# Performance work log

Measured on AMD Instinct MI355X. Metric: run time of the kernel, lower is better.

Reference implementation:

```python
import jax, jax.numpy as jnp
import numpy as np

H = 768   # hidden (cell) size
P = 256   # projection size
I = 80    # input feature dim
L = 3     # model_num_layers
B, T = 256, 400


def setup_inputs() -> dict:
    key = jax.random.key(0)
    ks = jax.random.split(key, 16)
    s = 0.05
    inp = {"x": jax.random.normal(ks[0], (B, T, I), dtype=jnp.float32)}
    in_dims = [I, P, P]
    for l in range(L):
        inp[f"Wx{l}"] = jax.random.normal(ks[1 + 4 * l], (in_dims[l], 4 * H), dtype=jnp.float32) * s
        inp[f"Wh{l}"] = jax.random.normal(ks[2 + 4 * l], (P, 4 * H), dtype=jnp.float32) * s
        inp[f"b{l}"] = jnp.zeros((4 * H,), dtype=jnp.float32)
        inp[f"Wp{l}"] = jax.random.normal(ks[3 + 4 * l], (H, P), dtype=jnp.float32) * s
    inp["W"] = jax.random.normal(ks[13], (P, P), dtype=jnp.float32) * s
    inp["lb"] = jnp.zeros((P,), dtype=jnp.float32)
    return inp


def _lstmp_layer(x, Wx, Wh, b, Wp, c0, h0):
    # Precompute input contribution to gates: [B, T, 4H]
    xg = jnp.einsum("bti,ig->btg", x, Wx) + b

    def step(carry, xg_t):
        c, h = carry
        gates = xg_t + h @ Wh              # [B, 4H]
        i, f, g, o = jnp.split(gates, 4, axis=-1)
        i = jax.nn.sigmoid(i)
        f = jax.nn.sigmoid(f)
        g = jnp.tanh(g)
        o = jax.nn.sigmoid(o)
        c = f * c + i * g                  # [B, H]
        h = (o * jnp.tanh(c)) @ Wp         # [B, P] projected hidden
        return (c, h), h

    (c, h), hs = jax.lax.scan(step, (c0, h0), jnp.swapaxes(xg, 0, 1))
    return jnp.swapaxes(hs, 0, 1), c, h   # seq_out [B,T,P], final c, h


def reference(x, Wx0, Wh0, b0, Wp0, Wx1, Wh1, b1, Wp1, Wx2, Wh2, b2, Wp2, W, lb):
    batch = x.shape[0]
    c = jnp.zeros((batch, H), dtype=x.dtype)
    h = jnp.zeros((batch, P), dtype=x.dtype)
    seq = x
    params = [(Wx0, Wh0, b0, Wp0), (Wx1, Wh1, b1, Wp1), (Wx2, Wh2, b2, Wp2)]
    for (Wx, Wh, b, Wp) in params:
        seq, c, h = _lstmp_layer(seq, Wx, Wh, b, Wp, c, h)
    embeds_raw = jax.nn.relu(seq.mean(axis=1) @ W.T + lb)   # [B, P]
    norm = jnp.linalg.norm(embeds_raw, axis=1, keepdims=True)
    return embeds_raw / norm
```

## Files before the change

### kernel.cpp

```cpp
#include <hip/hip_runtime.h>
#include <cstdint>
#include <cstddef>


typedef __attribute__((ext_vector_type(8))) short bf16x8;
typedef __attribute__((ext_vector_type(4))) float f32x4;
typedef __attribute__((ext_vector_type(2))) int i32x2;

#define TT 400
#define NB 256
#define IIP 96
#define HH 768
#define PP 256
#define G4 3072
#define WGJ 48
#define SMEMB (131072 + 2048)

__device__ __forceinline__ short f2bf(float f) {
  unsigned u = __builtin_bit_cast(unsigned, f);
  unsigned r = u + 0x7FFFu + ((u >> 16) & 1u);
  return (short)(r >> 16);
}
__device__ __forceinline__ float sigf(float x) { return 1.0f / (1.0f + __expf(-x)); }
__device__ __forceinline__ float tanh_(float x) { return 1.0f - 2.0f / (__expf(2.0f * x) + 1.0f); }

__device__ __forceinline__ void st_co_b64(void* p, i32x2 v) {
  asm volatile("global_store_dwordx2 %0, %1, off sc0 sc1" :: "v"(p), "v"(v) : "memory");
}
__device__ __forceinline__ int ld_flag(const int* p) {
  int v;
  asm volatile("global_load_dword %0, %1, off sc0 sc1\n\ts_waitcnt vmcnt(0)"
               : "=v"(v) : "v"(p) : "memory");
  return v;
}


__global__ void k_xb(const float* __restrict__ x, short* __restrict__ xb) {
  int idx = blockIdx.x * 256 + threadIdx.x;
  if (idx >= TT * NB * 80) return;
  int i = idx % 80, tb = idx / 80;
  int b = tb % NB, t = tb / NB;
  xb[(size_t)(t * NB + b) * IIP + i] = f2bf(x[(size_t)(b * TT + t) * 80 + i]);
}

__global__ void k_makeB(const float* __restrict__ Wx, const float* __restrict__ Wp,
                        const float* __restrict__ Wh, short* __restrict__ out,
                        int K, int KIN, int INDIM) {
  int np = blockIdx.x * 256 + threadIdx.x;
  int k = blockIdx.y;
  int j2 = np >> 6, wj = np & 63, ntg = wj >> 4, cc = wj & 15;
  int col = ntg * HH + j2 * 16 + cc;
  float v;
  if (k < KIN) {
    v = (k < INDIM) ? Wx[(size_t)k * G4 + col] : 0.0f;
  } else {
    float a = 0.f;
    int kr = k - KIN;
    for (int q = 0; q < PP; ++q)
      a = fmaf(Wp[(size_t)kr * PP + q], Wh[(size_t)q * G4 + col], a);
    v = a;
  }
  out[(size_t)np * K + k] = f2bf(v);
}

__global__ void k_wpT(const float* __restrict__ Wp, short* __restrict__ WpT) {
  int idx = blockIdx.x * 256 + threadIdx.x;
  if (idx >= PP * HH) return;
  int n = idx % PP, k = idx / PP;
  WpT[(size_t)n * HH + k] = f2bf(Wp[(size_t)k * PP + n]);
}

__global__ void k_whT(const float* __restrict__ Wh, short* __restrict__ WhT) {
  int idx = blockIdx.x * 256 + threadIdx.x;
  if (idx >= G4 * PP) return;
  int np = idx % G4, k = idx / G4;
  int j2 = np >> 6, wj = np & 63, ntg = wj >> 4, cc = wj & 15;
  int col = ntg * HH + j2 * 16 + cc;
  WhT[(size_t)np * PP + k] = f2bf(Wh[(size_t)k * G4 + col]);
}

__global__ void k_pb(const float* b0, const float* b1, const float* b2, float* pb) {
  int n = blockIdx.x * 256 + threadIdx.x;
  if (n >= 3 * G4) return;
  int l = n / G4, np = n % G4;
  int j2 = np >> 6, wj = np & 63, ntg = wj >> 4, cc = wj & 15;
  int col = ntg * HH + j2 * 16 + cc;
  pb[n] = (l == 0 ? b0 : (l == 1 ? b1 : b2))[col];
}

__global__ void k_wt(const float* __restrict__ W, float* __restrict__ Wt) {
  int idx = blockIdx.x * 256 + threadIdx.x;
  int q = idx >> 8, p = idx & 255;
  Wt[idx] = W[p * 256 + q];
}

__global__ void __launch_bounds__(256) k_trans2(
    const short* __restrict__ seqF,
    const short* __restrict__ WhT, float* __restrict__ xg0b)
{
  const int blk = blockIdx.x;
  const int g = blk & 3, j = blk >> 2;
  const int tid = threadIdx.x, lane = tid & 63, wv = tid >> 6;
  const int c0 = lane & 15, rg = lane >> 4;
  const int row0 = g * 64;
  const short* aseq = seqF + (size_t)(row0 + wv * 16 + c0) * PP + rg * 8;

  f32x4 zz = {0.f, 0.f, 0.f, 0.f};
  f32x4 acc[4];
  #pragma unroll
  for (int nt = 0; nt < 4; ++nt) acc[nt] = zz;
  #pragma unroll
  for (int c = 0; c < 8; ++c) {
    bf16x8 a = *(const bf16x8*)(aseq + c * 32);
    #pragma unroll
    for (int nt = 0; nt < 4; ++nt) {
      bf16x8 b = *(const bf16x8*)(WhT + (size_t)(j * 64 + nt * 16 + c0) * PP + c * 32 + rg * 8);
      acc[nt] = __builtin_amdgcn_mfma_f32_16x16x32_bf16(a, b, acc[nt], 0, 0, 0);
    }
  }
  #pragma unroll
  for (int nt = 0; nt < 4; ++nt)
    #pragma unroll
    for (int r = 0; r < 4; ++r)
      xg0b[(size_t)(row0 + wv * 16 + rg * 4 + r) * G4 + j * 64 + nt * 16 + c0] = acc[nt][r];
}


__device__ __forceinline__ void bar_arrive(int* cnt, int tid) {
  asm volatile("s_waitcnt vmcnt(0)" ::: "memory");
  __syncthreads();
  if (tid == 0) {
    int old = __hip_atomic_fetch_add(cnt, 1, __ATOMIC_RELAXED, __HIP_MEMORY_SCOPE_AGENT);
    (void)old;
  }
}
__device__ __forceinline__ void bar_wait(const int* cnt, int wv, int target) {
  if (wv == 0) {
    while (ld_flag(cnt) < target) __builtin_amdgcn_s_sleep(2);
    __builtin_amdgcn_fence(__ATOMIC_ACQUIRE, "agent");
  }
  __syncthreads();
}


template <int K>
__device__ __forceinline__ void stageB(const short* __restrict__ Bw, char* BsC, int j, int tid) {
  const char* src = (const char*)(Bw + (size_t)j * 64 * K);
  constexpr int UPR = K / 8;
  constexpr int ITERS = 64 * UPR / 256;
  #pragma unroll
  for (int it = 0; it < ITERS; ++it) {
    int u = it * 256 + tid;
    int wj = u / UPR;
    int k0 = (u - wj * UPR) * 8;
    bf16x8 v = *(const bf16x8*)(src + (size_t)wj * (K * 2) + k0 * 2);
    int gi = ((k0 >> 3) ^ (wj >> 1)) & 3;
    *(bf16x8*)(BsC + ((k0 >> 5) << 12) + (wj << 6) + (gi << 4)) = v;
  }
}


template <int CIN, int DOPROJ, int DOSUM, int USEXG>
__global__ void __launch_bounds__(256, 1) k_layer(
    const short* __restrict__ Bw,
    const short* __restrict__ inS, const int inStr,
    const short* __restrict__ WpT, short* __restrict__ projOut,
    const float* __restrict__ pbL,
    short* __restrict__ U, float* __restrict__ Cw, float* __restrict__ S,
    const float* __restrict__ xg0b, int* __restrict__ cntBase)
{
  extern __shared__ char smem[];
  char* BsC = smem;
  short* UtS = (short*)(smem + 131072);
  const int bx = blockIdx.x;
  const int xcd = bx & 7;
  const int g = xcd >> 1;
  const int j = (xcd & 1) * 24 + (bx >> 3);
  const int tid = threadIdx.x;
  const int lane = tid & 63, wv = tid >> 6, c0 = lane & 15, rg = lane >> 4;
  const int row0 = g * 64;
  int* cnt = (int*)((char*)cntBase + g * 4096);
  constexpr int K = CIN * 32 + 768;

  stageB<K>(Bw, BsC, j, tid);

  float creg[4], sreg[4] = {0.f, 0.f, 0.f, 0.f};
  #pragma unroll
  for (int r = 0; r < 4; ++r)
    creg[r] = USEXG ? Cw[(size_t)(row0 + wv * 16 + rg * 4 + r) * HH + j * 16 + c0] : 0.f;

  float bias[4];
  int fbB[4];
  #pragma unroll
  for (int nt = 0; nt < 4; ++nt) {
    bias[nt] = pbL[j * 64 + nt * 16 + c0];
    fbB[nt] = ((nt * 16 + c0) << 6) | (((rg ^ (c0 >> 1)) & 3) << 4);
  }
  const short* wb = DOPROJ ? (WpT + (size_t)(j * 16 + c0) * HH + rg * 8) : nullptr;
  f32x4 zz = {0.f, 0.f, 0.f, 0.f};

  __syncthreads();

  for (int t = 0; t < TT; ++t) {
    const int pw = t & 1, pr = pw ^ 1;
    const short* aX = inS + (size_t)t * NB * inStr + (size_t)(row0 + wv * 16 + c0) * inStr + rg * 8;
    const short* aU = U + (size_t)pr * NB * HH + (size_t)(row0 + wv * 16 + c0) * HH + rg * 8;

    f32x4 acc[4];
    if (USEXG && t == 0) {
      #pragma unroll
      for (int nt = 0; nt < 4; ++nt)
        #pragma unroll
        for (int r = 0; r < 4; ++r)
          acc[nt][r] = xg0b[(size_t)(row0 + wv * 16 + rg * 4 + r) * G4 + j * 64 + nt * 16 + c0];
    } else {
      #pragma unroll
      for (int nt = 0; nt < 4; ++nt) acc[nt] = zz;
    }

    bf16x8 xf[CIN];
    #pragma unroll
    for (int c = 0; c < CIN; ++c) xf[c] = *(const bf16x8*)(aX + c * 32);
    #pragma unroll
    for (int c = 0; c < CIN; ++c)
      #pragma unroll
      for (int nt = 0; nt < 4; ++nt)
        acc[nt] = __builtin_amdgcn_mfma_f32_16x16x32_bf16(
            xf[c], *(const bf16x8*)(BsC + (c << 12) + fbB[nt]), acc[nt], 0, 0, 0);

    bf16x8 uf[24];
    if (t > 0) {
      bar_wait(cnt, wv, WGJ * t);
      #pragma unroll
      for (int c = 0; c < 24; ++c) uf[c] = *(const bf16x8*)(aU + c * 32);
      #pragma unroll
      for (int c = 0; c < 24; ++c)
        #pragma unroll
        for (int nt = 0; nt < 4; ++nt)
          acc[nt] = __builtin_amdgcn_mfma_f32_16x16x32_bf16(
              uf[c], *(const bf16x8*)(BsC + ((CIN + c) << 12) + fbB[nt]), acc[nt], 0, 0, 0);
    }

    #pragma unroll
    for (int r = 0; r < 4; ++r) {
      float gi = acc[0][r] + bias[0];
      float gf = acc[1][r] + bias[1];
      float gg = acc[2][r] + bias[2];
      float go = acc[3][r] + bias[3];
      float cc2 = sigf(gf) * creg[r] + sigf(gi) * tanh_(gg);
      creg[r] = cc2;
      float uu = sigf(go) * tanh_(cc2);
      if (DOSUM) sreg[r] += uu;
      UtS[(wv * 16 + rg * 4 + r) * 16 + c0] = f2bf(uu);
    }
    __syncthreads();
    {
      int row = tid >> 2, q = tid & 3;
      i32x2 v = *(const i32x2*)(UtS + row * 16 + q * 4);
      st_co_b64((short*)U + (size_t)pw * NB * HH + (size_t)(row0 + row) * HH + j * 16 + q * 4, v);
    }
    bar_arrive(cnt, tid);

    if (DOPROJ && j < 16 && t > 0) {
      f32x4 pacc = zz;
      #pragma unroll
      for (int c = 0; c < 24; ++c)
        pacc = __builtin_amdgcn_mfma_f32_16x16x32_bf16(
            uf[c], *(const bf16x8*)(wb + c * 32), pacc, 0, 0, 0);
      #pragma unroll
      for (int r = 0; r < 4; ++r)
        UtS[(wv * 16 + rg * 4 + r) * 16 + c0] = f2bf(pacc[r]);
      __syncthreads();
      int row = tid >> 2, q = tid & 3;
      i32x2 v = *(const i32x2*)(UtS + row * 16 + q * 4);
      st_co_b64(projOut + (size_t)(t - 1) * NB * PP + (size_t)(row0 + row) * PP + j * 16 + q * 4, v);
    }
  }

  bar_wait(cnt, wv, WGJ * TT);
  if (DOPROJ && j < 16) {
    const short* aU1 = U + (size_t)1 * NB * HH + (size_t)(row0 + wv * 16 + c0) * HH + rg * 8;
    f32x4 pacc = zz;
    #pragma unroll
    for (int c = 0; c < 24; ++c) {
      bf16x8 a = *(const bf16x8*)(aU1 + c * 32);
      pacc = __builtin_amdgcn_mfma_f32_16x16x32_bf16(a, *(const bf16x8*)(wb + c * 32), pacc, 0, 0, 0);
    }
    #pragma unroll
    for (int r = 0; r < 4; ++r)
      UtS[(wv * 16 + rg * 4 + r) * 16 + c0] = f2bf(pacc[r]);
    __syncthreads();
    int row = tid >> 2, q = tid & 3;
    i32x2 v = *(const i32x2*)(UtS + row * 16 + q * 4);
    st_co_b64(projOut + (size_t)399 * NB * PP + (size_t)(row0 + row) * PP + j * 16 + q * 4, v);
  }

  #pragma unroll
  for (int r = 0; r < 4; ++r) {
    size_t idx = (size_t)(row0 + wv * 16 + rg * 4 + r) * HH + j * 16 + c0;
    Cw[idx] = creg[r];
    if (DOSUM) S[idx] = sreg[r];
  }
}


__global__ void k_mh(const float* __restrict__ S, const float* __restrict__ Wp2, float* __restrict__ mh) {
  __shared__ float sl[HH];
  int b = blockIdx.x, p = threadIdx.x;
  for (int i = p; i < HH; i += 256) sl[i] = S[(size_t)b * HH + i] * (1.0f / 400.0f);
  __syncthreads();
  float a = 0.f;
  for (int k = 0; k < HH; ++k) a = fmaf(sl[k], Wp2[(size_t)k * PP + p], a);
  mh[b * PP + p] = a;
}

__global__ void k_out(const float* __restrict__ mh, const float* __restrict__ Wt,
                      const float* __restrict__ lb, float* __restrict__ out) {
  __shared__ float ml[PP];
  __shared__ float red[PP];
  int b = blockIdx.x, p = threadIdx.x;
  ml[p] = mh[b * PP + p];
  __syncthreads();
  float z = lb[p];
  for (int q = 0; q < PP; ++q) z = fmaf(ml[q], Wt[q * PP + p], z);
  z = fmaxf(z, 0.0f);
  red[p] = z * z;
  __syncthreads();
  for (int st = 128; st > 0; st >>= 1) { if (p < st) red[p] += red[p + st]; __syncthreads(); }
  out[b * PP + p] = z / sqrtf(red[0]);
}


extern "C" void kernel_launch(void* const* d_in, const int* in_sizes, int n_in,
                              void* d_out, int out_size, void* d_ws, size_t ws_size,
                              hipStream_t stream) {
  (void)in_sizes; (void)n_in; (void)out_size; (void)ws_size;
  const float* x   = (const float*)d_in[0];
  const float* Wx0 = (const float*)d_in[1];
  const float* Wh0 = (const float*)d_in[2];
  const float* b0  = (const float*)d_in[3];
  const float* Wp0 = (const float*)d_in[4];
  const float* Wx1 = (const float*)d_in[5];
  const float* Wh1 = (const float*)d_in[6];
  const float* b1  = (const float*)d_in[7];
  const float* Wp1 = (const float*)d_in[8];
  const float* Wx2 = (const float*)d_in[9];
  const float* Wh2 = (const float*)d_in[10];
  const float* b2  = (const float*)d_in[11];
  const float* Wp2 = (const float*)d_in[12];
  const float* W   = (const float*)d_in[13];
  const float* lb  = (const float*)d_in[14];

  char* w = (char*)d_ws;
  auto take = [&](size_t bytes) { char* p = w; w += (bytes + 4095) & ~(size_t)4095; return p; };
  short* xb    = (short*)take((size_t)TT * NB * IIP * 2);
  short* B0w   = (short*)take((size_t)G4 * 864 * 2);
  short* B1w   = (short*)take((size_t)G4 * 1024 * 2);
  short* B2w   = (short*)take((size_t)G4 * 1024 * 2);
  float* pbw   = (float*)take((size_t)3 * G4 * 4);
  short* WpT0  = (short*)take((size_t)PP * HH * 2);
  short* WpT1  = (short*)take((size_t)PP * HH * 2);
  short* WhT1  = (short*)take((size_t)G4 * PP * 2);
  short* WhT2  = (short*)take((size_t)G4 * PP * 2);
  short* U     = (short*)take((size_t)2 * NB * HH * 2);
  short* seqH  = (short*)take((size_t)TT * NB * PP * 2);
  float* xg0b  = (float*)take((size_t)NB * G4 * 4);
  float* Cw    = (float*)take((size_t)NB * HH * 4);
  float* Sw    = (float*)take((size_t)NB * HH * 4);
  float* mhw   = (float*)take((size_t)NB * PP * 4);
  float* Wtw   = (float*)take((size_t)PP * PP * 4);
  int*   cnts  = (int*)take(3 * 4 * 4096);

  hipMemsetAsync(xb, 0, (size_t)TT * NB * IIP * 2, stream);
  hipMemsetAsync(cnts, 0, 3 * 4 * 4096, stream);

  k_xb<<<(TT * NB * 80 + 255) / 256, 256, 0, stream>>>(x, xb);
  k_makeB<<<dim3(12, 864), 256, 0, stream>>>(Wx0, Wp0, Wh0, B0w, 864, 96, 80);
  k_makeB<<<dim3(12, 1024), 256, 0, stream>>>(Wx1, Wp1, Wh1, B1w, 1024, 256, 256);
  k_makeB<<<dim3(12, 1024), 256, 0, stream>>>(Wx2, Wp2, Wh2, B2w, 1024, 256, 256);
  k_wpT<<<(PP * HH + 255) / 256, 256, 0, stream>>>(Wp0, WpT0);
  k_wpT<<<(PP * HH + 255) / 256, 256, 0, stream>>>(Wp1, WpT1);
  k_whT<<<(G4 * PP + 255) / 256, 256, 0, stream>>>(Wh1, WhT1);
  k_whT<<<(G4 * PP + 255) / 256, 256, 0, stream>>>(Wh2, WhT2);
  k_pb<<<(3 * G4 + 255) / 256, 256, 0, stream>>>(b0, b1, b2, pbw);
  k_wt<<<(PP * PP) / 256, 256, 0, stream>>>(W, Wtw);

  hipFuncSetAttribute((const void*)k_layer<3, 1, 0, 0>,
                      hipFuncAttributeMaxDynamicSharedMemorySize, SMEMB);
  hipFuncSetAttribute((const void*)k_layer<8, 1, 0, 1>,
                      hipFuncAttributeMaxDynamicSharedMemorySize, SMEMB);
  hipFuncSetAttribute((const void*)k_layer<8, 0, 1, 1>,
                      hipFuncAttributeMaxDynamicSharedMemorySize, SMEMB);

  k_layer<3, 1, 0, 0><<<4 * WGJ, 256, SMEMB, stream>>>(
      B0w, xb, IIP, WpT0, seqH, pbw + 0 * G4, U, Cw, Sw, xg0b,
      (int*)((char*)cnts + 0 * 16384));
  k_trans2<<<4 * WGJ, 256, 0, stream>>>(seqH + (size_t)399 * NB * PP, WhT1, xg0b);

  k_layer<8, 1, 0, 1><<<4 * WGJ, 256, SMEMB, stream>>>(
      B1w, seqH, PP, WpT1, seqH, pbw + 1 * G4, U, Cw, Sw, xg0b,
      (int*)((char*)cnts + 1 * 16384));
  k_trans2<<<4 * WGJ, 256, 0, stream>>>(seqH + (size_t)399 * NB * PP, WhT2, xg0b);

  k_layer<8, 0, 1, 1><<<4 * WGJ, 256, SMEMB, stream>>>(
      B2w, seqH, PP, nullptr, nullptr, pbw + 2 * G4, U, Cw, Sw, xg0b,
      (int*)((char*)cnts + 2 * 16384));

  k_mh<<<NB, 256, 0, stream>>>(Sw, Wp2, mhw);
  k_out<<<NB, 256, 0, stream>>>(mhw, Wtw, lb, (float*)d_out);
}
```

Baseline: 11.29 ms.

## Use XCD-aware cache scope for recurrent state loads, drop acquire fence

Each workgroup publishes its hardware XCC id at kernel start. Workgroups then build a mask of which 32-column chunks of the recurrent state were produced on the same XCC, and load those chunks with sc0 only so they can hit the local L2, while remote chunks still bypass with sc0 sc1. The state is also written with a normal store next to the coherent one, the projection output uses plain stores, and the acquire fence after the barrier spin is removed. This aims to cut per-step latency in the serial 400-step loop. It relies on undocumented cache-coherence behaviour and adds a startup handshake, plus a second xccp buffer that is reused by all three launches and never reset.

```diff
diff --git a/kernel.cpp b/kernel.cpp
--- a/kernel.cpp
+++ b/kernel.cpp
@@ -14,7 +14,7 @@
 #define PP 256
 #define G4 3072
 #define WGJ 48
-#define SMEMB (131072 + 2048)
+#define SMEMB (131072 + 2048 + 64)
 
 __device__ __forceinline__ short f2bf(float f) {
   unsigned u = __builtin_bit_cast(unsigned, f);
@@ -26,6 +26,9 @@
 
 __device__ __forceinline__ void st_co_b64(void* p, i32x2 v) {
   asm volatile("global_store_dwordx2 %0, %1, off sc0 sc1" :: "v"(p), "v"(v) : "memory");
+}
+__device__ __forceinline__ void st_co_b32(void* p, int v) {
+  asm volatile("global_store_dword %0, %1, off sc0 sc1" :: "v"(p), "v"(v) : "memory");
 }
 __device__ __forceinline__ int ld_flag(const int* p) {
   int v;
@@ -33,6 +36,27 @@
                : "=v"(v) : "v"(p) : "memory");
   return v;
 }
+__device__ __forceinline__ bf16x8 ld_sc0(const void* p) {
+  bf16x8 v;
+  asm volatile("global_load_dwordx4 %0, %1, off sc0" : "=v"(v) : "v"(p));
+  return v;
+}
+__device__ __forceinline__ bf16x8 ld_sc01(const void* p) {
+  bf16x8 v;
+  asm volatile("global_load_dwordx4 %0, %1, off sc0 sc1" : "=v"(v) : "v"(p));
+  return v;
+}
+__device__ __forceinline__ int get_xcc() {
+  int x;
+  asm("s_getreg_b32 %0, hwreg(HW_REG_XCC_ID)" : "=s"(x));
+  return x & 15;
+}
+#define WAIT_TIE24(u) \
+  asm volatile("s_waitcnt vmcnt(0)" \
+    : "+v"(u[0]),"+v"(u[1]),"+v"(u[2]),"+v"(u[3]),"+v"(u[4]),"+v"(u[5]), \
+      "+v"(u[6]),"+v"(u[7]),"+v"(u[8]),"+v"(u[9]),"+v"(u[10]),"+v"(u[11]), \
+      "+v"(u[12]),"+v"(u[13]),"+v"(u[14]),"+v"(u[15]),"+v"(u[16]),"+v"(u[17]), \
+      "+v"(u[18]),"+v"(u[19]),"+v"(u[20]),"+v"(u[21]),"+v"(u[22]),"+v"(u[23]))
 
 
 __global__ void k_xb(const float* __restrict__ x, short* __restrict__ xb) {
@@ -129,15 +153,12 @@
 __device__ __forceinline__ void bar_arrive(int* cnt, int tid) {
   asm volatile("s_waitcnt vmcnt(0)" ::: "memory");
   __syncthreads();
-  if (tid == 0) {
-    int old = __hip_atomic_fetch_add(cnt, 1, __ATOMIC_RELAXED, __HIP_MEMORY_SCOPE_AGENT);
-    (void)old;
-  }
+  if (tid == 0)
+    __hip_atomic_fetch_add(cnt, 1, __ATOMIC_RELAXED, __HIP_MEMORY_SCOPE_AGENT);
 }
 __device__ __forceinline__ void bar_wait(const int* cnt, int wv, int target) {
   if (wv == 0) {
     while (ld_flag(cnt) < target) __builtin_amdgcn_s_sleep(2);
-    __builtin_amdgcn_fence(__ATOMIC_ACQUIRE, "agent");
   }
   __syncthreads();
 }
@@ -167,11 +188,13 @@
     const short* __restrict__ WpT, short* __restrict__ projOut,
     const float* __restrict__ pbL,
     short* __restrict__ U, float* __restrict__ Cw, float* __restrict__ S,
-    const float* __restrict__ xg0b, int* __restrict__ cntBase)
+    const float* __restrict__ xg0b, int* __restrict__ cntBase,
+    int* __restrict__ xccp)
 {
   extern __shared__ char smem[];
   char* BsC = smem;
   short* UtS = (short*)(smem + 131072);
+  char* xccL = smem + 131072 + 2048;
   const int bx = blockIdx.x;
   const int xcd = bx & 7;
   const int g = xcd >> 1;
@@ -179,10 +202,33 @@
   const int tid = threadIdx.x;
   const int lane = tid & 63, wv = tid >> 6, c0 = lane & 15, rg = lane >> 4;
   const int row0 = g * 64;
-  int* cnt = (int*)((char*)cntBase + g * 4096);
+  int* cnt  = (int*)((char*)cntBase + g * 4096);
+  int* cntX = cnt + 256;
+  int* xpub = xccp + g * 64;
+  const int myxcc = get_xcc();
   constexpr int K = CIN * 32 + 768;
 
+  if (tid == 0) st_co_b32(xpub + j, myxcc);
+  asm volatile("s_waitcnt vmcnt(0)" ::: "memory");
+  __syncthreads();
+  if (tid == 0)
+    __hip_atomic_fetch_add(cntX, 1, __ATOMIC_RELAXED, __HIP_MEMORY_SCOPE_AGENT);
+
   stageB<K>(Bw, BsC, j, tid);
+
+  if (wv == 0) {
+    while (ld_flag(cntX) < WGJ) __builtin_amdgcn_s_sleep(2);
+    if (lane < WGJ) {
+      int v = ld_flag(xpub + lane);
+      xccL[lane] = (char)v;
+    }
+  }
+  __syncthreads();
+  unsigned cmask = 0;
+  for (int c = 0; c < 24; ++c)
+    if (xccL[2 * c] == (char)myxcc && xccL[2 * c + 1] == (char)myxcc)
+      cmask |= (1u << c);
+  cmask = __builtin_amdgcn_readfirstlane(cmask);
 
   float creg[4], sreg[4] = {0.f, 0.f, 0.f, 0.f};
   #pragma unroll
@@ -232,7 +278,11 @@
     if (t > 0) {
       bar_wait(cnt, wv, WGJ * t);
       #pragma unroll
-      for (int c = 0; c < 24; ++c) uf[c] = *(const bf16x8*)(aU + c * 32);
+      for (int c = 0; c < 24; ++c) {
+        const void* p = aU + c * 32;
+        uf[c] = ((cmask >> c) & 1) ? ld_sc0(p) : ld_sc01(p);
+      }
+      WAIT_TIE24(uf);
       #pragma unroll
       for (int c = 0; c < 24; ++c)
         #pragma unroll
@@ -257,7 +307,9 @@
     {
       int row = tid >> 2, q = tid & 3;
       i32x2 v = *(const i32x2*)(UtS + row * 16 + q * 4);
-      st_co_b64((short*)U + (size_t)pw * NB * HH + (size_t)(row0 + row) * HH + j * 16 + q * 4, v);
+      short* dst = (short*)U + (size_t)pw * NB * HH + (size_t)(row0 + row) * HH + j * 16 + q * 4;
+      *(i32x2*)dst = v;
+      st_co_b64(dst, v);
     }
     bar_arrive(cnt, tid);
 
@@ -273,7 +325,7 @@
       __syncthreads();
       int row = tid >> 2, q = tid & 3;
       i32x2 v = *(const i32x2*)(UtS + row * 16 + q * 4);
-      st_co_b64(projOut + (size_t)(t - 1) * NB * PP + (size_t)(row0 + row) * PP + j * 16 + q * 4, v);
+      *(i32x2*)(projOut + (size_t)(t - 1) * NB * PP + (size_t)(row0 + row) * PP + j * 16 + q * 4) = v;
     }
   }
 
@@ -283,7 +335,8 @@
     f32x4 pacc = zz;
     #pragma unroll
     for (int c = 0; c < 24; ++c) {
-      bf16x8 a = *(const bf16x8*)(aU1 + c * 32);
+      bf16x8 a = ((cmask >> c) & 1) ? ld_sc0(aU1 + c * 32) : ld_sc01(aU1 + c * 32);
+      asm volatile("s_waitcnt vmcnt(0)" : "+v"(a));
       pacc = __builtin_amdgcn_mfma_f32_16x16x32_bf16(a, *(const bf16x8*)(wb + c * 32), pacc, 0, 0, 0);
     }
     #pragma unroll
@@ -292,7 +345,7 @@
     __syncthreads();
     int row = tid >> 2, q = tid & 3;
     i32x2 v = *(const i32x2*)(UtS + row * 16 + q * 4);
-    st_co_b64(projOut + (size_t)399 * NB * PP + (size_t)(row0 + row) * PP + j * 16 + q * 4, v);
+    *(i32x2*)(projOut + (size_t)399 * NB * PP + (size_t)(row0 + row) * PP + j * 16 + q * 4) = v;
   }
 
   #pragma unroll
@@ -370,6 +423,7 @@
   float* mhw   = (float*)take((size_t)NB * PP * 4);
   float* Wtw   = (float*)take((size_t)PP * PP * 4);
   int*   cnts  = (int*)take(3 * 4 * 4096);
+  int*   xccp  = (int*)take(4 * 64 * 4);
 
   hipMemsetAsync(xb, 0, (size_t)TT * NB * IIP * 2, stream);
   hipMemsetAsync(cnts, 0, 3 * 4 * 4096, stream);
@@ -394,17 +448,17 @@
 
   k_layer<3, 1, 0, 0><<<4 * WGJ, 256, SMEMB, stream>>>(
       B0w, xb, IIP, WpT0, seqH, pbw + 0 * G4, U, Cw, Sw, xg0b,
-      (int*)((char*)cnts + 0 * 16384));
+      (int*)((char*)cnts + 0 * 16384), xccp);
   k_trans2<<<4 * WGJ, 256, 0, stream>>>(seqH + (size_t)399 * NB * PP, WhT1, xg0b);
 
   k_layer<8, 1, 0, 1><<<4 * WGJ, 256, SMEMB, stream>>>(
       B1w, seqH, PP, WpT1, seqH, pbw + 1 * G4, U, Cw, Sw, xg0b,
-      (int*)((char*)cnts + 1 * 16384));
+      (int*)((char*)cnts + 1 * 16384), xccp);
   k_trans2<<<4 * WGJ, 256, 0, stream>>>(seqH + (size_t)399 * NB * PP, WhT2, xg0b);
 
   k_layer<8, 0, 1, 1><<<4 * WGJ, 256, SMEMB, stream>>>(
       B2w, seqH, PP, nullptr, nullptr, pbw + 2 * G4, U, Cw, Sw, xg0b,
-      (int*)((char*)cnts + 2 * 16384));
+      (int*)((char*)cnts + 2 * 16384), xccp);
 
   k_mh<<<NB, 256, 0, stream>>>(Sw, Wp2, mhw);
   k_out<<<NB, 256, 0, stream>>>(mhw, Wtw, lb, (float*)d_out);
```

New measurement: 15.52 ms. +37.4%, slower.
